# Kernel optimization log

Hardware: AMD Instinct MI355X
Metric: run time of the kernel (lower is better)

Reference implementation:

```python
import jax, jax.numpy as jnp
import numpy as np

NEIGHBOUR_NUM = 8  # args.neighbour_num


def _sqrdis_map(x, y):
    # x: [B,M,3], y: [B,N,3] -> [B,M,N] squared distances
    x2 = jnp.sum(x * x, axis=-1)
    y2 = jnp.sum(y * y, axis=-1)
    inner = jnp.einsum('bmd,bnd->bmn', x, y)
    return x2[:, :, None] + y2[:, None, :] - 2.0 * inner


def _chamfer(x, y):
    d = _sqrdis_map(x, y)
    return d.min(axis=2), d.min(axis=1)


def _neighbor_index(v, k):
    # torch.topk(dist, k+1, largest=False) then drop self
    d = _sqrdis_map(v, v)
    idx = jax.lax.top_k(-d, k + 1)[1]  # ascending distance order
    return idx[:, :, 1:]


def _arap(idx, dp, sp):
    B = dp.shape[0]
    bid = jnp.arange(B)[:, None, None]
    dn = dp[bid, idx] - dp[:, :, None, :]  # [B,N,K,3]
    sn = sp[bid, idx] - sp[:, :, None, :]
    dd = jnp.sqrt(jnp.sum(dn * dn, axis=-1) + 1e-5)
    sd = jnp.sqrt(jnp.sum(sn * sn, axis=-1) + 1e-5)
    diff = dd - sd
    return jnp.sum(diff * diff) / B


def setup_inputs() -> dict:
    key = jax.random.key(0)
    ks = jax.random.split(key, 7)
    T, B, N = 3, 4, 4096
    return {
        'phi': jax.random.normal(ks[0], (T, B, 1024), dtype=jnp.float32),
        'point_weight': jax.random.normal(ks[1], (T, B, N, 1), dtype=jnp.float32),
        'deform_rigid_points': 0.5 * jax.random.normal(ks[2], (T, B, N, 3), dtype=jnp.float32),
        'deformation_points': 0.5 * jax.random.normal(ks[3], (T, B, N, 3), dtype=jnp.float32),
        'rigid_matrix': 0.1 * jax.random.normal(ks[4], (T, B, 4, 4), dtype=jnp.float32),
        'source_points': jax.random.uniform(ks[5], (B, N, 3), dtype=jnp.float32, minval=-1.0, maxval=1.0),
        'target_points': jax.random.uniform(ks[6], (B, N, 3), dtype=jnp.float32, minval=-1.0, maxval=1.0),
    }


def reference(phi, point_weight, deform_rigid_points, deformation_points,
              rigid_matrix, source_points, target_points):
    B = source_points.shape[0]
    T = phi.shape[0]  # iter_time = len(phi_list)
    idx = _neighbor_index(source_points, NEIGHBOUR_NUM)
    trans_mask = jnp.zeros((4, 4), dtype=rigid_matrix.dtype).at[0:3, 3].set(1.0)
    total = jnp.asarray(0.0, dtype=source_points.dtype)
    for t in range(T):  # small fixed iter count, structurally distinct stages
        dp = deformation_points[t]
        # loss_on_cd
        d1, d2 = _chamfer(dp, target_points)
        cd = (jnp.sum(d1) + jnp.sum(d2)) * 0.5 / B
        # loss_on_pd (rigid-deformed vs full deformation)
        diff = deform_rigid_points[t] - dp
        pd = jnp.sum(diff * diff) / B
        # loss_on_sparse
        sp = jnp.mean(jnp.abs(point_weight[t]))
        # loss_on_tran
        tr = trans_mask[None] * rigid_matrix[t]
        tran = jnp.sum(tr * tr) / B
        # loss_on_arap
        ar = _arap(idx, dp, source_points)
        total = total + cd + pd + sp + tran + ar
    return total
```

## Files before the change

kernel.cpp:

```cpp
#include <hip/hip_runtime.h>

#define T_ 3
#define B_ 4
#define N_ 4096
#define K_ 8

#define KNN_BLOCKS (B_ * (N_ / 8))
#define CH_BLOCKS  (T_ * B_ * 2 * 16)
#define SL_BLOCKS  32
#define KWIN 1024
#define CWIN 512

typedef short bf16x8 __attribute__((ext_vector_type(8)));
typedef float f32x4  __attribute__((ext_vector_type(4)));

template <int NW>
__device__ inline float block_reduce(float v, float* scratch) {
    #pragma unroll
    for (int off = 32; off > 0; off >>= 1) v += __shfl_down(v, off, 64);
    const int lane = threadIdx.x & 63, wid = threadIdx.x >> 6;
    if (lane == 0) scratch[wid] = v;
    __syncthreads();
    float s = 0.f;
    if (threadIdx.x == 0) {
        #pragma unroll
        for (int w = 0; w < NW; ++w) s += scratch[w];
    }
    return s;
}

#define CE_(A, i, j) { unsigned lo_ = min(A[i], A[j]); A[j] = max(A[i], A[j]); A[i] = lo_; }
__device__ inline void sort8(unsigned s[8]) {
    CE_(s,0,1) CE_(s,2,3) CE_(s,4,5) CE_(s,6,7)
    CE_(s,0,2) CE_(s,1,3) CE_(s,4,6) CE_(s,5,7)
    CE_(s,1,2) CE_(s,5,6)
    CE_(s,0,4) CE_(s,1,5) CE_(s,2,6) CE_(s,3,7)
    CE_(s,2,4) CE_(s,3,5)
    CE_(s,1,2) CE_(s,3,4) CE_(s,5,6)
}
__device__ inline void merge_top8(unsigned a[8], const unsigned s[8]) {
    #pragma unroll
    for (int i = 0; i < 8; ++i) a[i] = min(a[i], s[7 - i]);
    CE_(a,0,4) CE_(a,1,5) CE_(a,2,6) CE_(a,3,7)
    CE_(a,0,2) CE_(a,1,3) CE_(a,4,6) CE_(a,5,7)
    CE_(a,0,1) CE_(a,2,3) CE_(a,4,5) CE_(a,6,7)
}

__device__ inline short hi16(float v) { return (short)(__float_as_uint(v) >> 16); }
__device__ inline float residual(float v) {
    return v - __uint_as_float(__float_as_uint(v) & 0xFFFF0000u);
}
__device__ inline unsigned pk2(short a, short b) {
    return (unsigned)(unsigned short)a | ((unsigned)(unsigned short)b << 16);
}
#define BF16_ONE ((short)0x3F80)

__global__ __launch_bounds__(256, 6) void mega_kernel(const float* __restrict__ src,
                                                      const float* __restrict__ dp_all,
                                                      const float* __restrict__ tp,
                                                      const float* __restrict__ drp,
                                                      const float* __restrict__ pw,
                                                      const float* __restrict__ rm,
                                                      float* __restrict__ out) {
    __shared__ uint4 smem4[1024];

    if (blockIdx.x < KNN_BLOCKS) {
        float4* win = (float4*)smem4;
        const int b  = blockIdx.x / (N_ / 8);
        const int q0 = (blockIdx.x % (N_ / 8)) * 8;
        const float* sb = src + (size_t)b * N_ * 3;

        const int wv = threadIdx.x >> 6;
        const int c  = threadIdx.x & 63;
        const int i0 = q0 + 2 * wv, i1 = i0 + 1;
        const float qx0 = sb[3 * i0], qy0 = sb[3 * i0 + 1], qz0 = sb[3 * i0 + 2];
        const float qx1 = sb[3 * i1], qy1 = sb[3 * i1 + 1], qz1 = sb[3 * i1 + 2];
        const float q20 = fmaf(qx0, qx0, fmaf(qy0, qy0, qz0 * qz0));
        const float q21 = fmaf(qx1, qx1, fmaf(qy1, qy1, qz1 * qz1));

        unsigned a0[K_], a1[K_];
        #pragma unroll
        for (int p = 0; p < K_; ++p) { a0[p] = 0xFFFFFFFFu; a1[p] = 0xFFFFFFFFu; }

        for (int w = 0; w < N_ / KWIN; ++w) {
            __syncthreads();
            for (int j = threadIdx.x; j < KWIN; j += 256) {
                int jg = w * KWIN + j;
                float x = sb[3 * jg], y = sb[3 * jg + 1], z = sb[3 * jg + 2];
                win[j] = make_float4(-2.f * x, -2.f * y, -2.f * z,
                                     fmaf(x, x, fmaf(y, y, z * z)));
            }
            __syncthreads();

            #pragma unroll
            for (int bt = 0; bt < KWIN / 8 / 64; ++bt) {
                unsigned s0[8], s1[8];
                #pragma unroll
                for (int u = 0; u < 8; ++u) {
                    int jl = 64 * (bt * 8 + u) + c;
                    float4 cd = win[jl];
                    int jglob = w * KWIN + jl;
                    float d0 = fmaf(qx0, cd.x, fmaf(qy0, cd.y, fmaf(qz0, cd.z, cd.w))) + q20;
                    float d1 = fmaf(qx1, cd.x, fmaf(qy1, cd.y, fmaf(qz1, cd.z, cd.w))) + q21;
                    unsigned p0 = (__float_as_uint(d0) & 0xFFFFF000u) | (unsigned)jglob;
                    unsigned p1 = (__float_as_uint(d1) & 0xFFFFF000u) | (unsigned)jglob;
                    s0[u] = (jglob == i0) ? 0xFFFFFFFFu : p0;
                    s1[u] = (jglob == i1) ? 0xFFFFFFFFu : p1;
                }
                sort8(s0); merge_top8(a0, s0);
                sort8(s1); merge_top8(a1, s1);
            }
        }

        #pragma unroll
        for (int mask = 32; mask >= 1; mask >>= 1) {
            unsigned t0[8], t1[8];
            #pragma unroll
            for (int e = 0; e < K_; ++e) {
                t0[e] = __shfl_xor(a0[e], mask, 64);
                t1[e] = __shfl_xor(a1[e], mask, 64);
            }
            merge_top8(a0, t0);
            merge_top8(a1, t1);
        }

        __syncthreads();
        unsigned* nidx = (unsigned*)smem4 + 64;
        if (c == 0) {
            #pragma unroll
            for (int e = 0; e < K_; ++e) {
                nidx[(2 * wv) * K_ + e]     = a0[e] & 0xFFFu;
                nidx[(2 * wv + 1) * K_ + e] = a1[e] & 0xFFFu;
            }
        }
        __syncthreads();

        float acc = 0.f;
        if (threadIdx.x < 8 * K_) {
            const int q  = threadIdx.x >> 3;
            const int qi = q0 + q;
            const int j  = (int)nidx[threadIdx.x];
            float sx = sb[3 * qi], sy = sb[3 * qi + 1], sz = sb[3 * qi + 2];
            float ex = sb[3 * j] - sx, ey = sb[3 * j + 1] - sy, ez = sb[3 * j + 2] - sz;
            float sd = sqrtf(fmaf(ex, ex, fmaf(ey, ey, ez * ez)) + 1e-5f);
            #pragma unroll
            for (int t = 0; t < T_; ++t) {
                const float* dpb = dp_all + ((size_t)(t * B_ + b)) * N_ * 3;
                float dx = dpb[3 * j] - dpb[3 * qi];
                float dy = dpb[3 * j + 1] - dpb[3 * qi + 1];
                float dz = dpb[3 * j + 2] - dpb[3 * qi + 2];
                float dd = sqrtf(fmaf(dx, dx, fmaf(dy, dy, dz * dz)) + 1e-5f);
                float df = dd - sd;
                acc = fmaf(df, df, acc);
            }
        }
        float s = block_reduce<4>(acc, (float*)smem4);
        if (threadIdx.x == 0) atomicAdd(out, s * (1.0f / B_));

    } else if (blockIdx.x < KNN_BLOCKS + CH_BLOCKS) {
        uint4* alds = smem4;
        const int cb   = blockIdx.x - KNN_BLOCKS;
        const int tbd  = cb >> 4;
        const int slab = cb & 15;
        const int dir = tbd & 1;
        const int tb  = tbd >> 1;
        const int b = tb % B_, t = tb / B_;

        const float* dpb = dp_all + ((size_t)(t * B_ + b)) * N_ * 3;
        const float* tpb = tp + (size_t)b * N_ * 3;
        const float* cbase = dir ? dpb : tpb;
        const float* qbase = dir ? tpb : dpb;

        const int lane = threadIdx.x & 63;
        const int wave = threadIdx.x >> 6;
        const int quad = lane >> 4;
        const int n    = lane & 15;

        bf16x8 bfrag[4];
        float  q2r[4];
        #pragma unroll
        for (int s = 0; s < 4; ++s) {
            int qid = slab * 256 + wave * 64 + s * 16 + n;
            float x = qbase[3 * qid], y = qbase[3 * qid + 1], z = qbase[3 * qid + 2];
            q2r[s] = fmaf(x, x, fmaf(y, y, z * z));
            short hx = hi16(x), hy = hi16(y), hz = hi16(z);
            short lx = hi16(residual(x)), ly = hi16(residual(y)), lz = hi16(residual(z));
            if (quad == 0)
                bfrag[s] = (bf16x8){hx, hy, hz, hx, hy, hz, BF16_ONE, BF16_ONE};
            else if (quad == 1)
                bfrag[s] = (bf16x8){lx, ly, lz, lx, ly, lz, 0, 0};
            else
                bfrag[s] = (bf16x8)(short)0;
        }

        float run[4] = {3.4e38f, 3.4e38f, 3.4e38f, 3.4e38f};
        const f32x4 zero4 = {0.f, 0.f, 0.f, 0.f};

        for (int w = 0; w < N_ / CWIN; ++w) {
            __syncthreads();
            #pragma unroll
            for (int r = 0; r < 2; ++r) {
                int jloc = r * 256 + threadIdx.x;
                int jg = w * CWIN + jloc;
                float x = cbase[3 * jg], y = cbase[3 * jg + 1], z = cbase[3 * jg + 2];
                float p2 = fmaf(x, x, fmaf(y, y, z * z));
                float mx = -2.f * x, my = -2.f * y, mz = -2.f * z;
                short mhx = hi16(mx), mhy = hi16(my), mhz = hi16(mz);
                short mlx = hi16(residual(mx)), mly = hi16(residual(my)), mlz = hi16(residual(mz));
                short p2h = hi16(p2), p2l = hi16(residual(p2));
                uint4 f0 = make_uint4(pk2(mhx, mhy), pk2(mhz, mlx), pk2(mly, mlz), pk2(p2h, p2l));
                uint4 f1 = make_uint4(f0.x, f0.y, f0.z, 0u);
                int tile = jloc >> 4, m = jloc & 15;
                alds[tile * 32 + m]      = f0;
                alds[tile * 32 + 16 + m] = f1;
            }
            __syncthreads();

            #pragma unroll 4
            for (int tile = 0; tile < CWIN / 16; ++tile) {
                bf16x8 af = (bf16x8)(short)0;
                if (quad < 2) {
                    union { uint4 u; bf16x8 v; } cv;
                    cv.u = alds[tile * 32 + quad * 16 + n];
                    af = cv.v;
                }
                #pragma unroll
                for (int s = 0; s < 4; ++s) {
                    f32x4 d = __builtin_amdgcn_mfma_f32_16x16x32_bf16(af, bfrag[s], zero4, 0, 0, 0);
                    float r3 = fminf(fminf(d[0], d[1]), d[2]);
                    run[s] = fminf(fminf(run[s], r3), d[3]);
                }
            }
        }

        float vsum = 0.f;
        #pragma unroll
        for (int s = 0; s < 4; ++s) {
            float r = run[s];
            r = fminf(r, __shfl_xor(r, 32));
            r = fminf(r, __shfl_xor(r, 16));
            if (lane < 16) vsum += r + q2r[s];
        }
        __syncthreads();
        float ssum = block_reduce<4>(vsum, (float*)smem4);
        if (threadIdx.x == 0) atomicAdd(out, ssum * (0.5f / B_));

    } else {
        const int PD_N = T_ * B_ * N_ * 3;
        const int SP_N = T_ * B_ * N_;
        const int stride = SL_BLOCKS * 256;
        const int gid = (blockIdx.x - KNN_BLOCKS - CH_BLOCKS) * 256 + threadIdx.x;
        float apd = 0.f;
        for (int i = gid; i < PD_N; i += stride) {
            float d = drp[i] - dp_all[i];
            apd = fmaf(d, d, apd);
        }
        float asp = 0.f;
        for (int i = gid; i < SP_N; i += stride) asp += fabsf(pw[i]);
        float atr = 0.f;
        if (gid < T_ * B_ * 3) {
            int t = gid / (B_ * 3);
            int b = (gid / 3) % B_;
            int r = gid % 3;
            float v = rm[t * B_ * 16 + b * 16 + r * 4 + 3];
            atr = v * v;
        }
        float acc = apd * (1.0f / B_) + asp * (1.0f / (B_ * N_)) + atr * (1.0f / B_);
        float s = block_reduce<4>(acc, (float*)smem4);
        if (threadIdx.x == 0) atomicAdd(out, s);
    }
}

extern "C" void kernel_launch(void* const* d_in, const int* in_sizes, int n_in,
                              void* d_out, int out_size, void* d_ws, size_t ws_size,
                              hipStream_t stream) {
    const float* pw  = (const float*)d_in[1];
    const float* drp = (const float*)d_in[2];
    const float* dp  = (const float*)d_in[3];
    const float* rm  = (const float*)d_in[4];
    const float* sp  = (const float*)d_in[5];
    const float* tp  = (const float*)d_in[6];
    float* out = (float*)d_out;

    hipMemsetAsync(out, 0, sizeof(float), stream);
    mega_kernel<<<KNN_BLOCKS + CH_BLOCKS + SL_BLOCKS, 256, 0, stream>>>(
        sp, dp, tp, drp, pw, rm, out);
}
```

Baseline: 134.6 us.

## Compute KNN distance tiles with bf16x3 MFMA instead of scalar FMA

The KNN stage now builds its 16-query by 16-candidate squared-distance tiles with MFMA bf16 instructions, using a hi/lo split for precision, in place of per-lane scalar FMAs. Each block handles 16 queries, and each wave scans a quarter of every 512-point window. Per-lane top-8 lists are merged across quads by shuffles and then across waves through shared memory. This moves distance arithmetic off the vector ALU, and it changes work distribution, block count and the neighbour-merge structure. The bf16 hi/lo split may slightly perturb distance ties.

Result: faster. 124.6 us (-7.4%).

```diff
diff --git a/kernel.cpp b/kernel.cpp
--- a/kernel.cpp
+++ b/kernel.cpp
@@ -5,10 +5,9 @@
 #define N_ 4096
 #define K_ 8
 
-#define KNN_BLOCKS (B_ * (N_ / 8))
+#define KNN_BLOCKS (B_ * (N_ / 16))
 #define CH_BLOCKS  (T_ * B_ * 2 * 16)
 #define SL_BLOCKS  32
-#define KWIN 1024
 #define CWIN 512
 
 typedef short bf16x8 __attribute__((ext_vector_type(8)));
@@ -63,82 +62,122 @@
                                                       const float* __restrict__ rm,
                                                       float* __restrict__ out) {
     __shared__ uint4 smem4[1024];
+    const f32x4 zero4 = {0.f, 0.f, 0.f, 0.f};
 
     if (blockIdx.x < KNN_BLOCKS) {
-        float4* win = (float4*)smem4;
-        const int b  = blockIdx.x / (N_ / 8);
-        const int q0 = (blockIdx.x % (N_ / 8)) * 8;
+        uint4* alds = smem4;
+        const int b   = blockIdx.x / (N_ / 16);
+        const int qt0 = (blockIdx.x % (N_ / 16)) * 16;
         const float* sb = src + (size_t)b * N_ * 3;
 
-        const int wv = threadIdx.x >> 6;
-        const int c  = threadIdx.x & 63;
-        const int i0 = q0 + 2 * wv, i1 = i0 + 1;
-        const float qx0 = sb[3 * i0], qy0 = sb[3 * i0 + 1], qz0 = sb[3 * i0 + 2];
-        const float qx1 = sb[3 * i1], qy1 = sb[3 * i1 + 1], qz1 = sb[3 * i1 + 2];
-        const float q20 = fmaf(qx0, qx0, fmaf(qy0, qy0, qz0 * qz0));
-        const float q21 = fmaf(qx1, qx1, fmaf(qy1, qy1, qz1 * qz1));
-
-        unsigned a0[K_], a1[K_];
-        #pragma unroll
-        for (int p = 0; p < K_; ++p) { a0[p] = 0xFFFFFFFFu; a1[p] = 0xFFFFFFFFu; }
-
-        for (int w = 0; w < N_ / KWIN; ++w) {
+        const int wid  = __builtin_amdgcn_readfirstlane(threadIdx.x >> 6);
+        const int lane = threadIdx.x & 63;
+        const int n    = lane & 15;
+        const int quad = lane >> 4;
+        const int rbase = quad * 4;
+        const int qid  = qt0 + n;
+
+        bf16x8 bfrag = (bf16x8)(short)0;
+        {
+            float x = sb[3 * qid], y = sb[3 * qid + 1], z = sb[3 * qid + 2];
+            float q2 = fmaf(x, x, fmaf(y, y, z * z));
+            short hx = hi16(x), hy = hi16(y), hz = hi16(z);
+            short lx = hi16(residual(x)), ly = hi16(residual(y)), lz = hi16(residual(z));
+            if (quad == 0) bfrag = (bf16x8){hx, hy, hz, hx, hy, hz, BF16_ONE, BF16_ONE};
+            else if (quad == 1) bfrag = (bf16x8){lx, ly, lz, lx, ly, lz,
+                                                 hi16(q2), hi16(residual(q2))};
+        }
+
+        unsigned a[K_];
+        #pragma unroll
+        for (int p = 0; p < K_; ++p) a[p] = 0xFFFFFFFFu;
+
+        for (int w = 0; w < N_ / CWIN; ++w) {
             __syncthreads();
-            for (int j = threadIdx.x; j < KWIN; j += 256) {
-                int jg = w * KWIN + j;
+            #pragma unroll
+            for (int r = 0; r < 2; ++r) {
+                int jloc = r * 256 + threadIdx.x;
+                int jg = w * CWIN + jloc;
                 float x = sb[3 * jg], y = sb[3 * jg + 1], z = sb[3 * jg + 2];
-                win[j] = make_float4(-2.f * x, -2.f * y, -2.f * z,
-                                     fmaf(x, x, fmaf(y, y, z * z)));
+                float p2 = fmaf(x, x, fmaf(y, y, z * z));
+                float mx = -2.f * x, my = -2.f * y, mz = -2.f * z;
+                short mhx = hi16(mx), mhy = hi16(my), mhz = hi16(mz);
+                short mlx = hi16(residual(mx)), mly = hi16(residual(my)), mlz = hi16(residual(mz));
+                uint4 f0 = make_uint4(pk2(mhx, mhy), pk2(mhz, mlx), pk2(mly, mlz),
+                                      pk2(hi16(p2), hi16(residual(p2))));
+                uint4 f1 = make_uint4(f0.x, f0.y, f0.z, pk2(BF16_ONE, BF16_ONE));
+                int tile = jloc >> 4, m = jloc & 15;
+                alds[tile * 32 + m]      = f0;
+                alds[tile * 32 + 16 + m] = f1;
             }
             __syncthreads();
 
             #pragma unroll
-            for (int bt = 0; bt < KWIN / 8 / 64; ++bt) {
-                unsigned s0[8], s1[8];
+            for (int bt = 0; bt < 4; ++bt) {
+                unsigned s8[8];
                 #pragma unroll
-                for (int u = 0; u < 8; ++u) {
-                    int jl = 64 * (bt * 8 + u) + c;
-                    float4 cd = win[jl];
-                    int jglob = w * KWIN + jl;
-                    float d0 = fmaf(qx0, cd.x, fmaf(qy0, cd.y, fmaf(qz0, cd.z, cd.w))) + q20;
-                    float d1 = fmaf(qx1, cd.x, fmaf(qy1, cd.y, fmaf(qz1, cd.z, cd.w))) + q21;
-                    unsigned p0 = (__float_as_uint(d0) & 0xFFFFF000u) | (unsigned)jglob;
-                    unsigned p1 = (__float_as_uint(d1) & 0xFFFFF000u) | (unsigned)jglob;
-                    s0[u] = (jglob == i0) ? 0xFFFFFFFFu : p0;
-                    s1[u] = (jglob == i1) ? 0xFFFFFFFFu : p1;
+                for (int h = 0; h < 2; ++h) {
+                    const int tile = wid * 8 + bt * 2 + h;
+                    const int tbg  = w * CWIN + tile * 16;
+                    bf16x8 af = (bf16x8)(short)0;
+                    if (quad < 2) {
+                        union { uint4 u; bf16x8 v; } cv;
+                        cv.u = alds[tile * 32 + quad * 16 + n];
+                        af = cv.v;
+                    }
+                    f32x4 d = __builtin_amdgcn_mfma_f32_16x16x32_bf16(af, bfrag, zero4, 0, 0, 0);
+                    #pragma unroll
+                    for (int r = 0; r < 4; ++r)
+                        s8[h * 4 + r] = (__float_as_uint(d[r]) & 0xFFFFF000u)
+                                        | (unsigned)(tbg | (rbase + r));
+                    if (tbg == qt0) {
+                        #pragma unroll
+                        for (int r = 0; r < 4; ++r)
+                            if (rbase + r == n) s8[h * 4 + r] = 0xFFFFFFFFu;
+                    }
                 }
-                sort8(s0); merge_top8(a0, s0);
-                sort8(s1); merge_top8(a1, s1);
-            }
-        }
-
-        #pragma unroll
-        for (int mask = 32; mask >= 1; mask >>= 1) {
-            unsigned t0[8], t1[8];
-            #pragma unroll
-            for (int e = 0; e < K_; ++e) {
-                t0[e] = __shfl_xor(a0[e], mask, 64);
-                t1[e] = __shfl_xor(a1[e], mask, 64);
-            }
-            merge_top8(a0, t0);
-            merge_top8(a1, t1);
+                sort8(s8);
+                merge_top8(a, s8);
+            }
+        }
+
+        #pragma unroll
+        for (int mk = 16; mk <= 32; mk <<= 1) {
+            unsigned t[8];
+            #pragma unroll
+            for (int e = 0; e < K_; ++e) t[e] = __shfl_xor(a[e], mk, 64);
+            merge_top8(a, t);
         }
 
         __syncthreads();
-        unsigned* nidx = (unsigned*)smem4 + 64;
-        if (c == 0) {
-            #pragma unroll
-            for (int e = 0; e < K_; ++e) {
-                nidx[(2 * wv) * K_ + e]     = a0[e] & 0xFFFu;
-                nidx[(2 * wv + 1) * K_ + e] = a1[e] & 0xFFFu;
-            }
+        unsigned* sm = (unsigned*)smem4;
+        unsigned* nidx = (unsigned*)smem4 + 1024;
+        if (lane < 16) {
+            #pragma unroll
+            for (int e = 0; e < K_; ++e) sm[(wid * 16 + n) * 9 + e] = a[e];
         }
         __syncthreads();
+        if (threadIdx.x < 16) {
+            const int q = threadIdx.x;
+            unsigned md[K_];
+            #pragma unroll
+            for (int e = 0; e < K_; ++e) md[e] = sm[q * 9 + e];
+            #pragma unroll
+            for (int wv = 1; wv < 4; ++wv) {
+                unsigned t[8];
+                #pragma unroll
+                for (int e = 0; e < K_; ++e) t[e] = sm[(wv * 16 + q) * 9 + e];
+                merge_top8(md, t);
+            }
+            #pragma unroll
+            for (int e = 0; e < K_; ++e) nidx[q * 8 + e] = md[e] & 0xFFFu;
+        }
+        __syncthreads();
 
         float acc = 0.f;
-        if (threadIdx.x < 8 * K_) {
+        if (threadIdx.x < 16 * K_) {
             const int q  = threadIdx.x >> 3;
-            const int qi = q0 + q;
+            const int qi = qt0 + q;
             const int j  = (int)nidx[threadIdx.x];
             float sx = sb[3 * qi], sy = sb[3 * qi + 1], sz = sb[3 * qi + 2];
             float ex = sb[3 * j] - sx, ey = sb[3 * j + 1] - sy, ez = sb[3 * j + 2] - sz;
@@ -194,7 +233,6 @@
         }
 
         float run[4] = {3.4e38f, 3.4e38f, 3.4e38f, 3.4e38f};
-        const f32x4 zero4 = {0.f, 0.f, 0.f, 0.f};
 
         for (int w = 0; w < N_ / CWIN; ++w) {
             __syncthreads();
@@ -207,8 +245,8 @@
                 float mx = -2.f * x, my = -2.f * y, mz = -2.f * z;
                 short mhx = hi16(mx), mhy = hi16(my), mhz = hi16(mz);
                 short mlx = hi16(residual(mx)), mly = hi16(residual(my)), mlz = hi16(residual(mz));
-                short p2h = hi16(p2), p2l = hi16(residual(p2));
-                uint4 f0 = make_uint4(pk2(mhx, mhy), pk2(mhz, mlx), pk2(mly, mlz), pk2(p2h, p2l));
+                uint4 f0 = make_uint4(pk2(mhx, mhy), pk2(mhz, mlx), pk2(mly, mlz),
+                                      pk2(hi16(p2), hi16(residual(p2))));
                 uint4 f1 = make_uint4(f0.x, f0.y, f0.z, 0u);
                 int tile = jloc >> 4, m = jloc & 15;
                 alds[tile * 32 + m]      = f0;
```
